# Kernel optimization log

Measured on AMD Instinct MI355X. Metric: run time of the kernel, lower is better.

## Reference

```python
import jax, jax.numpy as jnp
import numpy as np

K = 64
PI = np.float32(np.pi)


def setup_inputs() -> dict:
    key = jax.random.key(0)
    k1, k2 = jax.random.split(key)
    B, N = 4096, 21
    rotation = jax.random.normal(k1, (B, N, 3, 3), dtype=jnp.float32)
    conditions = jax.random.normal(k2, (B, N, 4 * K), dtype=jnp.float32)
    permute = np.arange(3).astype(np.int64)  # static permutation indices
    return {"rotation": rotation, "conditions": conditions, "permute": permute}


def _mobius_forward(rotation, conditions, p0, p1, p2):
    B, N = rotation.shape[0], rotation.shape[1]
    I3 = jnp.eye(3, dtype=rotation.dtype)

    x = rotation[..., p0]  # [B,N,3]
    y = rotation[..., p1]  # [B,N,3]

    # compute_mcl_parameters_nd
    weights = conditions[..., :K]                      # [B,N,K]
    w = conditions[..., K:].reshape(B, N, K, 3)        # [B,N,K,3]
    proj = I3 - jnp.einsum('bni,bnj->bnij', y, y)      # [B,N,3,3]
    w = jnp.einsum('bnij,bnkj->bnki', proj, w)
    r = -x
    r = r / jnp.linalg.norm(r, axis=-1, keepdims=True)
    v = jnp.cross(y, r)
    v = v / jnp.linalg.norm(v, axis=-1, keepdims=True)
    weights = jax.nn.softplus(weights)
    weights = weights / jnp.sum(weights, axis=-1, keepdims=True)
    w_norm = jnp.linalg.norm(w, axis=-1, keepdims=True)
    w = 0.7 / (1.0 + w_norm) * w

    # _forward_nd
    z = x
    zw = z[:, :, None, :] - w                          # [B,N,K,3]
    zw_norm = jnp.linalg.norm(zw, axis=-1)             # [B,N,K]
    w_norm2 = jnp.sum(w * w, axis=-1)                  # [B,N,K]
    h_z = ((1.0 - w_norm2) / zw_norm ** 2)[..., None] * zw - w  # [B,N,K,3]

    radians = jnp.arctan2(jnp.einsum('bnki,bni->bnk', h_z, v),
                          jnp.einsum('bnki,bni->bnk', h_z, r))
    ang = jnp.where(radians >= 0, radians, radians + 2.0 * PI)
    ang = jnp.sum(weights * ang, axis=2, keepdims=True)          # [B,N,1]
    tx = r * jnp.cos(ang) + v * jnp.sin(ang)                     # [B,N,3]

    zw_unit = zw / zw_norm[..., None]
    theta = jnp.arctan2(jnp.einsum('bni,bni->bn', x, v),
                        jnp.einsum('bni,bni->bn', x, r))[..., None]  # [B,N,1]
    dz_dtheta = -jnp.sin(theta) * r + jnp.cos(theta) * v             # [B,N,3]
    dh_dz = (1.0 - w_norm2)[..., None, None] * (
        I3 - 2.0 * jnp.einsum('bnki,bnkj->bnkij', zw_unit, zw_unit)
    ) / (zw_norm ** 2)[..., None, None]                              # [B,N,K,3,3]
    dh_dtheta = jnp.einsum('bnkpq,bnq->bnkp', dh_dz, dz_dtheta)      # [B,N,K,3]
    dtx = jnp.sum(jnp.linalg.norm(dh_dtheta, axis=-1) * weights, axis=2)  # [B,N]
    ldj = jnp.log(dtx)

    if (p1 - p0 == 1) or (p1 - p0 == -2):
        tz = jnp.cross(tx, y)
    else:
        tz = jnp.cross(y, tx)
    tz = tz / jnp.linalg.norm(tz, axis=-1, keepdims=True)

    cols = [None, None, None]
    cols[p0] = tx
    cols[p1] = y
    cols[p2] = tz
    trotation = jnp.stack(cols, axis=-1)  # [B,N,3,3]
    return trotation, jnp.sum(ldj, axis=-1)


def reference(rotation, conditions, permute):
    p0, p1, p2 = int(permute[0]), int(permute[1]), int(permute[2])
    return _mobius_forward(rotation, conditions, p0, p1, p2)
```

## Files before the change

### kernel.cpp

```cpp
#include <hip/hip_runtime.h>
#include <math.h>

#define PI_F    3.14159265358979323846f
#define TWO_PI  6.28318530717958647692f
#define HALF_PI 1.57079632679489661923f

__device__ __forceinline__ float frcp(float x)  { return __builtin_amdgcn_rcpf(x); }
__device__ __forceinline__ float frsq(float x)  { return __builtin_amdgcn_rsqf(x); }
__device__ __forceinline__ float fsqrt(float x) { return __builtin_amdgcn_sqrtf(x); }

__device__ __forceinline__ float fast_atan2_2pi(float y, float x) {
    float ax = fabsf(x), ay = fabsf(y);
    float mx = fmaxf(ax, ay), mn = fminf(ax, ay);
    float a  = (mx > 0.0f) ? mn * frcp(mx) : 0.0f;
    float s  = a * a;
    float r  = fmaf(s, fmaf(s, fmaf(s, fmaf(s, 0.0208351f, -0.085133f),
                                    0.180141f), -0.3302995f), 0.9998660f) * a;
    if (ay > ax) r = HALF_PI - r;
    if (x < 0.0f) r = PI_F - r;
    return (y < 0.0f) ? (TWO_PI - r) : r;
}

__global__ __launch_bounds__(448, 7)
void mobius_fwd(const float* __restrict__ rot,
                const float* __restrict__ cond,
                const void* __restrict__ perm,
                float* __restrict__ out,
                int B, int N)
{
    const int wave = threadIdx.x >> 6;
    const int lane = threadIdx.x & 63;
    const int sub  = lane >> 4;
    const int j    = lane & 15;
    const int nwav = blockDim.x >> 6;

    const int b0     = blockIdx.x * 4;
    const int nb     = min(4, B - b0);
    const int nit    = N * nb;
    const int nquads = (nit + 3) >> 2;

    const int* pi = (const int*)perm;
    int p0 = pi[0], p1 = pi[1], p2 = pi[2];
    bool pok = ((unsigned)p0 < 3u) && ((unsigned)p1 < 3u) && ((unsigned)p2 < 3u)
               && (p0 != p1) && (p0 != p2) && (p1 != p2);
    if (!pok) {
        const long long* pl = (const long long*)perm;
        p0 = (int)pl[0]; p1 = (int)pl[1]; p2 = (int)pl[2];
    }
    const int dd = p1 - p0;
    const bool swapc = (dd == 1 || dd == -2);

    __shared__ float s_ldj[128];

    const size_t base_item = (size_t)b0 * N;

    for (int q = wave; q < nquads; q += nwav) {
        const int  i0    = 4 * q + sub;
        const bool valid = (i0 < nit);
        const size_t item = base_item + (valid ? i0 : 0);

        const float* R = rot + item * 9;
        float x0 = R[p0], x1 = R[3 + p0], x2 = R[6 + p0];
        float y0 = R[p1], y1 = R[3 + p1], y2 = R[6 + p1];

        const float* C = cond + item * 256;
        float4 pw4 = *(const float4*)(C + 4 * j);
        float4 fa  = *(const float4*)(C + 64 + 12 * j);
        float4 fb  = *(const float4*)(C + 68 + 12 * j);
        float4 fc  = *(const float4*)(C + 72 + 12 * j);

        float xn2    = x0 * x0 + x1 * x1 + x2 * x2;
        float inv_xn = frsq(xn2);
        float xn     = xn2 * inv_xn;
        float xy     = x0 * y0 + x1 * y1 + x2 * y2;
        float yn2    = y0 * y0 + y1 * y1 + y2 * y2;
        float negA   = yn2 - 2.0f;

        float cv0 = x1 * y2 - x2 * y1;
        float cv1 = x2 * y0 - x0 * y2;
        float cv2 = x0 * y1 - x1 * y0;
        float inv_cn = frsq(cv0 * cv0 + cv1 * cv1 + cv2 * cv2);
        float v0 = cv0 * inv_cn, v1 = cv1 * inv_cn, v2 = cv2 * inv_cn;

        float PW[4] = {pw4.x, pw4.y, pw4.z, pw4.w};
        float W0[4] = {fa.x, fa.w, fb.z, fc.y};
        float W1[4] = {fa.y, fb.x, fb.w, fc.z};
        float W2[4] = {fa.z, fb.y, fc.x, fc.w};

        float pp = 0.0f, pa = 0.0f, pd = 0.0f;
        #pragma unroll
        for (int cc = 0; cc < 4; ++cc) {
            float w0 = W0[cc], w1 = W1[cc], w2 = W2[cc];
            float yw  = y0 * w0 + y1 * w1 + y2 * w2;
            float wp2 = w0 * w0 + w1 * w1 + w2 * w2;
            float xwp = x0 * w0 + x1 * w1 + x2 * w2;
            float vwp = v0 * w0 + v1 * w1 + v2 * w2;
            float qn  = fmaxf(fmaf(yw * yw, negA, wp2), 0.0f);
            float sc  = 0.7f * frcp(1.0f + fsqrt(qn));
            float wn2 = (sc * sc) * qn;
            float xw  = sc * fmaf(-xy, yw, xwp);
            float zwn2 = fmaf(-2.0f, xw, xn2 + wn2);
            float c   = (1.0f - wn2) * frcp(zwn2);
            float cp1 = c + 1.0f;
            float hv  = -(cp1 * (sc * vwp));
            float hr  = fmaf(cp1, xw * inv_xn, -(c * xn));
            float ang = fast_atan2_2pi(hv, hr);
            float p   = __logf(1.0f + __expf(PW[cc]));
            pp += p; pa = fmaf(p, ang, pa); pd = fmaf(p, c, pd);
        }

        #pragma unroll
        for (int off = 8; off >= 1; off >>= 1) {
            pp += __shfl_xor(pp, off, 64);
            pa += __shfl_xor(pa, off, 64);
            pd += __shfl_xor(pd, off, 64);
        }

        float ip   = frcp(pp);
        float angT = pa * ip;
        float ldj  = __logf(pd * ip);

        float sa, ca;
        __sincosf(angT, &sa, &ca);
        float r0 = -x0 * inv_xn, r1 = -x1 * inv_xn, r2 = -x2 * inv_xn;
        float t0 = fmaf(r0, ca, v0 * sa);
        float t1 = fmaf(r1, ca, v1 * sa);
        float t2 = fmaf(r2, ca, v2 * sa);

        float u0, u1, u2;
        if (swapc) {
            u0 = t1 * y2 - t2 * y1;
            u1 = t2 * y0 - t0 * y2;
            u2 = t0 * y1 - t1 * y0;
        } else {
            u0 = y1 * t2 - y2 * t1;
            u1 = y2 * t0 - y0 * t2;
            u2 = y0 * t1 - y1 * t0;
        }
        float iun = frsq(u0 * u0 + u1 * u1 + u2 * u2);
        u0 *= iun; u1 *= iun; u2 *= iun;

        if (valid) {
            if (j < 9) {
                int row = (j >= 6) ? 2 : (j >= 3) ? 1 : 0;
                int cp  = j - 3 * row;
                float tr = (row == 0) ? t0 : (row == 1) ? t1 : t2;
                float yr = (row == 0) ? y0 : (row == 1) ? y1 : y2;
                float ur = (row == 0) ? u0 : (row == 1) ? u1 : u2;
                float val = (cp == p0) ? tr : (cp == p1) ? yr : ur;
                out[item * 9 + j] = val;
            }
            if (j == 0) s_ldj[i0] = ldj;
        }
    }

    __syncthreads();
    if (threadIdx.x < nb) {
        float acc = 0.0f;
        for (int n = 0; n < N; ++n) acc += s_ldj[threadIdx.x * N + n];
        out[(size_t)B * N * 9 + b0 + threadIdx.x] = acc;
    }
}

extern "C" void kernel_launch(void* const* d_in, const int* in_sizes, int n_in,
                              void* d_out, int out_size, void* d_ws, size_t ws_size,
                              hipStream_t stream) {
    const float* rot  = (const float*)d_in[0];
    const float* cond = (const float*)d_in[1];
    const void*  perm = d_in[2];
    float* out = (float*)d_out;

    int items = in_sizes[0] / 9;
    int B = out_size - items * 9;
    int N = items / B;

    int grid = (B + 3) / 4;
    mobius_fwd<<<dim3(grid), dim3(448), 0, stream>>>(rot, cond, perm, out, B, N);
}
```

Measured before the change: 26.80 us.

## Double-buffer condition loads into LDS via async global_load_lds prefetch

Stages the per-item weight vectors (192 floats) into a per-wave double-buffered LDS region with asynchronous global-to-LDS loads, and prefetches the next quad's rotation and pre-weights into registers while the current quad computes. The aim is to hide global memory latency behind the math in a memory-bound kernel. In exchange it uses about 44KB of LDS per block, which may lower occupancy, drops the min-blocks launch bound, and relies on hand-placed vmcnt waits that must match the number of outstanding loads.

Measured after the change: 30.44 us. 1.14x slower.

```diff
diff --git a/kernel.cpp b/kernel.cpp
--- a/kernel.cpp
+++ b/kernel.cpp
@@ -8,6 +8,12 @@
 __device__ __forceinline__ float frcp(float x)  { return __builtin_amdgcn_rcpf(x); }
 __device__ __forceinline__ float frsq(float x)  { return __builtin_amdgcn_rsqf(x); }
 __device__ __forceinline__ float fsqrt(float x) { return __builtin_amdgcn_sqrtf(x); }
+
+__device__ __forceinline__ void glds16(const void* g, void* l) {
+    __builtin_amdgcn_global_load_lds(
+        (const __attribute__((address_space(1))) void*)g,
+        (__attribute__((address_space(3))) void*)l, 16, 0, 0);
+}
 
 __device__ __forceinline__ float fast_atan2_2pi(float y, float x) {
     float ax = fabsf(x), ay = fabsf(y);
@@ -21,7 +27,9 @@
     return (y < 0.0f) ? (TWO_PI - r) : r;
 }
 
-__global__ __launch_bounds__(448, 7)
+struct RotPW { float x0, x1, x2, y0, y1, y2; float4 pw; };
+
+__global__ __launch_bounds__(448)
 void mobius_fwd(const float* __restrict__ rot,
                 const float* __restrict__ cond,
                 const void* __restrict__ perm,
@@ -50,24 +58,59 @@
     const int dd = p1 - p0;
     const bool swapc = (dd == 1 || dd == -2);
 
+    __shared__ __align__(16) float cbuf[7][2][4][196];
     __shared__ float s_ldj[128];
 
     const size_t base_item = (size_t)b0 * N;
 
-    for (int q = wave; q < nquads; q += nwav) {
+    auto stage = [&](int par, int qq) {
+        if (lane < 48) {
+            #pragma unroll
+            for (int s = 0; s < 4; ++s) {
+                int iv = min(4 * qq + s, nit - 1);
+                const float* g = cond + (base_item + iv) * 256 + 64 + 4 * lane;
+                glds16(g, &cbuf[wave][par][s][0]);
+            }
+        }
+    };
+    auto loadrp = [&](RotPW& d, int qq) {
+        int iv = min(4 * qq + sub, nit - 1);
+        const float* R = rot + (base_item + iv) * 9;
+        d.x0 = R[p0]; d.x1 = R[3 + p0]; d.x2 = R[6 + p0];
+        d.y0 = R[p1]; d.y1 = R[3 + p1]; d.y2 = R[6 + p1];
+        d.pw = *(const float4*)(cond + (base_item + iv) * 256 + 4 * j);
+    };
+
+    RotPW cur{}, nxt{};
+    stage(0, wave);
+    loadrp(cur, wave);
+
+    int par = 0;
+    for (int q = wave; q < nquads; q += nwav, par ^= 1) {
+        const int qn = q + nwav;
+        const bool have_next = (qn < nquads);
+
+        if (have_next) {
+            stage(par ^ 1, qn);
+            asm volatile("s_waitcnt vmcnt(4)" ::: "memory");
+        } else {
+            asm volatile("s_waitcnt vmcnt(0)" ::: "memory");
+        }
+        __builtin_amdgcn_sched_barrier(0);
+
+        const float* myl = &cbuf[wave][par][sub][12 * j];
+        float4 fa = *(const float4*)(myl);
+        float4 fb = *(const float4*)(myl + 4);
+        float4 fc = *(const float4*)(myl + 8);
+
+        if (have_next) loadrp(nxt, qn);
+
         const int  i0    = 4 * q + sub;
         const bool valid = (i0 < nit);
         const size_t item = base_item + (valid ? i0 : 0);
 
-        const float* R = rot + item * 9;
-        float x0 = R[p0], x1 = R[3 + p0], x2 = R[6 + p0];
-        float y0 = R[p1], y1 = R[3 + p1], y2 = R[6 + p1];
-
-        const float* C = cond + item * 256;
-        float4 pw4 = *(const float4*)(C + 4 * j);
-        float4 fa  = *(const float4*)(C + 64 + 12 * j);
-        float4 fb  = *(const float4*)(C + 68 + 12 * j);
-        float4 fc  = *(const float4*)(C + 72 + 12 * j);
+        const float x0 = cur.x0, x1 = cur.x1, x2 = cur.x2;
+        const float y0 = cur.y0, y1 = cur.y1, y2 = cur.y2;
 
         float xn2    = x0 * x0 + x1 * x1 + x2 * x2;
         float inv_xn = frsq(xn2);
@@ -82,7 +125,7 @@
         float inv_cn = frsq(cv0 * cv0 + cv1 * cv1 + cv2 * cv2);
         float v0 = cv0 * inv_cn, v1 = cv1 * inv_cn, v2 = cv2 * inv_cn;
 
-        float PW[4] = {pw4.x, pw4.y, pw4.z, pw4.w};
+        float PW[4] = {cur.pw.x, cur.pw.y, cur.pw.z, cur.pw.w};
         float W0[4] = {fa.x, fa.w, fb.z, fc.y};
         float W1[4] = {fa.y, fb.x, fb.w, fc.z};
         float W2[4] = {fa.z, fb.y, fc.x, fc.w};
@@ -95,9 +138,9 @@
             float wp2 = w0 * w0 + w1 * w1 + w2 * w2;
             float xwp = x0 * w0 + x1 * w1 + x2 * w2;
             float vwp = v0 * w0 + v1 * w1 + v2 * w2;
-            float qn  = fmaxf(fmaf(yw * yw, negA, wp2), 0.0f);
-            float sc  = 0.7f * frcp(1.0f + fsqrt(qn));
-            float wn2 = (sc * sc) * qn;
+            float qn2 = fmaxf(fmaf(yw * yw, negA, wp2), 0.0f);
+            float sc  = 0.7f * frcp(1.0f + fsqrt(qn2));
+            float wn2 = (sc * sc) * qn2;
             float xw  = sc * fmaf(-xy, yw, xwp);
             float zwn2 = fmaf(-2.0f, xw, xn2 + wn2);
             float c   = (1.0f - wn2) * frcp(zwn2);
@@ -152,6 +195,8 @@
             }
             if (j == 0) s_ldj[i0] = ldj;
         }
+
+        cur = nxt;
     }
 
     __syncthreads();
```

## Process eight items per wave with eight K-components per lane

Applied to the files above, without the earlier changes.

Each lane now handles 8 of the 64 mixture components instead of 4, so a wave covers 8 items at once and each block covers 8 batch rows. The shuffle reduction gets one step shorter, and the per-item epilogue and output stores move to a single lane with scalar stores. The aim is to cut reduction and epilogue overhead per item and issue wider loads. In exchange, register pressure per lane goes up (launch bounds lowered to 4 blocks), the stores are serialized to one lane, and there are half as many blocks.

Result: faster. 25.66 us (-4.2%).

```diff
diff --git a/kernel.cpp b/kernel.cpp
--- a/kernel.cpp
+++ b/kernel.cpp
@@ -21,7 +21,7 @@
     return (y < 0.0f) ? (TWO_PI - r) : r;
 }
 
-__global__ __launch_bounds__(448, 7)
+__global__ __launch_bounds__(448, 4)
 void mobius_fwd(const float* __restrict__ rot,
                 const float* __restrict__ cond,
                 const void* __restrict__ perm,
@@ -30,14 +30,14 @@
 {
     const int wave = threadIdx.x >> 6;
     const int lane = threadIdx.x & 63;
-    const int sub  = lane >> 4;
-    const int j    = lane & 15;
+    const int sub  = lane >> 3;
+    const int j    = lane & 7;
     const int nwav = blockDim.x >> 6;
 
-    const int b0     = blockIdx.x * 4;
-    const int nb     = min(4, B - b0);
-    const int nit    = N * nb;
-    const int nquads = (nit + 3) >> 2;
+    const int b0   = blockIdx.x * 8;
+    const int nb   = min(8, B - b0);
+    const int nit  = N * nb;
+    const int noct = (nit + 7) >> 3;
 
     const int* pi = (const int*)perm;
     int p0 = pi[0], p1 = pi[1], p2 = pi[2];
@@ -50,24 +50,29 @@
     const int dd = p1 - p0;
     const bool swapc = (dd == 1 || dd == -2);
 
-    __shared__ float s_ldj[128];
+    __shared__ float s_ldj[192];
 
     const size_t base_item = (size_t)b0 * N;
 
-    for (int q = wave; q < nquads; q += nwav) {
-        const int  i0    = 4 * q + sub;
+    for (int q = wave; q < noct; q += nwav) {
+        const int  i0    = 8 * q + sub;
         const bool valid = (i0 < nit);
         const size_t item = base_item + (valid ? i0 : 0);
+
+        const float* C = cond + item * 256;
+        float4 pwa = *(const float4*)(C + 8 * j);
+        float4 pwb = *(const float4*)(C + 8 * j + 4);
+        const float* W = C + 64 + 24 * j;
+        float4 f0 = ((const float4*)W)[0];
+        float4 f1 = ((const float4*)W)[1];
+        float4 f2 = ((const float4*)W)[2];
+        float4 f3 = ((const float4*)W)[3];
+        float4 f4 = ((const float4*)W)[4];
+        float4 f5 = ((const float4*)W)[5];
 
         const float* R = rot + item * 9;
         float x0 = R[p0], x1 = R[3 + p0], x2 = R[6 + p0];
         float y0 = R[p1], y1 = R[3 + p1], y2 = R[6 + p1];
-
-        const float* C = cond + item * 256;
-        float4 pw4 = *(const float4*)(C + 4 * j);
-        float4 fa  = *(const float4*)(C + 64 + 12 * j);
-        float4 fb  = *(const float4*)(C + 68 + 12 * j);
-        float4 fc  = *(const float4*)(C + 72 + 12 * j);
 
         float xn2    = x0 * x0 + x1 * x1 + x2 * x2;
         float inv_xn = frsq(xn2);
@@ -82,22 +87,22 @@
         float inv_cn = frsq(cv0 * cv0 + cv1 * cv1 + cv2 * cv2);
         float v0 = cv0 * inv_cn, v1 = cv1 * inv_cn, v2 = cv2 * inv_cn;
 
-        float PW[4] = {pw4.x, pw4.y, pw4.z, pw4.w};
-        float W0[4] = {fa.x, fa.w, fb.z, fc.y};
-        float W1[4] = {fa.y, fb.x, fb.w, fc.z};
-        float W2[4] = {fa.z, fb.y, fc.x, fc.w};
+        float PW[8] = {pwa.x, pwa.y, pwa.z, pwa.w, pwb.x, pwb.y, pwb.z, pwb.w};
+        float W0[8] = {f0.x, f0.w, f1.z, f2.y, f3.x, f3.w, f4.z, f5.y};
+        float W1[8] = {f0.y, f1.x, f1.w, f2.z, f3.y, f4.x, f4.w, f5.z};
+        float W2[8] = {f0.z, f1.y, f2.x, f2.w, f3.z, f4.y, f5.x, f5.w};
 
         float pp = 0.0f, pa = 0.0f, pd = 0.0f;
         #pragma unroll
-        for (int cc = 0; cc < 4; ++cc) {
+        for (int cc = 0; cc < 8; ++cc) {
             float w0 = W0[cc], w1 = W1[cc], w2 = W2[cc];
             float yw  = y0 * w0 + y1 * w1 + y2 * w2;
             float wp2 = w0 * w0 + w1 * w1 + w2 * w2;
             float xwp = x0 * w0 + x1 * w1 + x2 * w2;
             float vwp = v0 * w0 + v1 * w1 + v2 * w2;
-            float qn  = fmaxf(fmaf(yw * yw, negA, wp2), 0.0f);
-            float sc  = 0.7f * frcp(1.0f + fsqrt(qn));
-            float wn2 = (sc * sc) * qn;
+            float qn2 = fmaxf(fmaf(yw * yw, negA, wp2), 0.0f);
+            float sc  = 0.7f * frcp(1.0f + fsqrt(qn2));
+            float wn2 = (sc * sc) * qn2;
             float xw  = sc * fmaf(-xy, yw, xwp);
             float zwn2 = fmaf(-2.0f, xw, xn2 + wn2);
             float c   = (1.0f - wn2) * frcp(zwn2);
@@ -110,47 +115,43 @@
         }
 
         #pragma unroll
-        for (int off = 8; off >= 1; off >>= 1) {
+        for (int off = 4; off >= 1; off >>= 1) {
             pp += __shfl_xor(pp, off, 64);
             pa += __shfl_xor(pa, off, 64);
             pd += __shfl_xor(pd, off, 64);
         }
 
-        float ip   = frcp(pp);
-        float angT = pa * ip;
-        float ldj  = __logf(pd * ip);
+        if (j == 0 && valid) {
+            float ip   = frcp(pp);
+            float angT = pa * ip;
+            float ldj  = __logf(pd * ip);
 
-        float sa, ca;
-        __sincosf(angT, &sa, &ca);
-        float r0 = -x0 * inv_xn, r1 = -x1 * inv_xn, r2 = -x2 * inv_xn;
-        float t0 = fmaf(r0, ca, v0 * sa);
-        float t1 = fmaf(r1, ca, v1 * sa);
-        float t2 = fmaf(r2, ca, v2 * sa);
+            float sa, ca;
+            __sincosf(angT, &sa, &ca);
+            float r0 = -x0 * inv_xn, r1 = -x1 * inv_xn, r2 = -x2 * inv_xn;
+            float t0 = fmaf(r0, ca, v0 * sa);
+            float t1 = fmaf(r1, ca, v1 * sa);
+            float t2 = fmaf(r2, ca, v2 * sa);
 
-        float u0, u1, u2;
-        if (swapc) {
-            u0 = t1 * y2 - t2 * y1;
-            u1 = t2 * y0 - t0 * y2;
-            u2 = t0 * y1 - t1 * y0;
-        } else {
-            u0 = y1 * t2 - y2 * t1;
-            u1 = y2 * t0 - y0 * t2;
-            u2 = y0 * t1 - y1 * t0;
-        }
-        float iun = frsq(u0 * u0 + u1 * u1 + u2 * u2);
-        u0 *= iun; u1 *= iun; u2 *= iun;
+            float u0, u1, u2;
+            if (swapc) {
+                u0 = t1 * y2 - t2 * y1;
+                u1 = t2 * y0 - t0 * y2;
+                u2 = t0 * y1 - t1 * y0;
+            } else {
+                u0 = y1 * t2 - y2 * t1;
+                u1 = y2 * t0 - y0 * t2;
+                u2 = y0 * t1 - y1 * t0;
+            }
+            float iun = frsq(u0 * u0 + u1 * u1 + u2 * u2);
+            u0 *= iun; u1 *= iun; u2 *= iun;
 
-        if (valid) {
-            if (j < 9) {
-                int row = (j >= 6) ? 2 : (j >= 3) ? 1 : 0;
-                int cp  = j - 3 * row;
-                float tr = (row == 0) ? t0 : (row == 1) ? t1 : t2;
-                float yr = (row == 0) ? y0 : (row == 1) ? y1 : y2;
-                float ur = (row == 0) ? u0 : (row == 1) ? u1 : u2;
-                float val = (cp == p0) ? tr : (cp == p1) ? yr : ur;
-                out[item * 9 + j] = val;
-            }
-            if (j == 0) s_ldj[i0] = ldj;
+            float* T = out + item * 9;
+            T[p0] = t0; T[3 + p0] = t1; T[6 + p0] = t2;
+            T[p1] = y0; T[3 + p1] = y1; T[6 + p1] = y2;
+            T[p2] = u0; T[3 + p2] = u1; T[6 + p2] = u2;
+
+            s_ldj[i0] = ldj;
         }
     }
 
@@ -174,6 +175,6 @@
     int B = out_size - items * 9;
     int N = items / B;
 
-    int grid = (B + 3) / 4;
+    int grid = (B + 7) / 8;
     mobius_fwd<<<dim3(grid), dim3(448), 0, stream>>>(rot, cond, perm, out, B, N);
 }
```
